# Performance work log

Hardware: AMD Instinct MI355X
Metric: run time of the kernel (lower is better)

Reference implementation:

```python
import jax, jax.numpy as jnp
import numpy as np

# Model dims (match init_kwargs)
B, S = 2, 2048
H = 1024          # hidden_size
I = 256           # intermediate_size
E = 256           # n_routed_experts
K = 8             # num_experts_per_tok
G = 8             # n_group
TG = 4            # topk_group
NS = 2            # n_shared_experts


def setup_inputs() -> dict:
    key = jax.random.key(0)
    ks = jax.random.split(key, 6)
    s = 0.02
    return {
        "x": jax.random.normal(ks[0], (B, S, H), jnp.float32),
        "Wg": jax.random.normal(ks[1], (E, H), jnp.float32) * s,          # gate Linear weight [E,H] (y = x @ Wg.T)
        "W_gate_up": jax.random.normal(ks[2], (E, H, 2 * I), jnp.float32) * s,  # per-expert gate_up proj
        "W_down": jax.random.normal(ks[3], (E, I, H), jnp.float32) * s,          # per-expert down proj
        "Ws_gate_up": jax.random.normal(ks[4], (NS, H, 2 * I), jnp.float32) * s, # shared experts
        "Ws_down": jax.random.normal(ks[5], (NS, I, H), jnp.float32) * s,
    }


def _mlp(x, w_gu, w_d):
    # DeepSeekV3 MLP: down( silu(gate) * up ); gate/up are the two chunks of gate_up
    gu = x @ w_gu                      # [N, 2I]
    g, u = gu[..., :I], gu[..., I:]
    return (jax.nn.silu(g) * u) @ w_d  # [N, H]


def reference(x, Wg, W_gate_up, W_down, Ws_gate_up, Ws_down):
    b, s, h = x.shape
    xf = x.reshape(-1, h)              # [N, H]
    n = xf.shape[0]

    # ---- shared experts (always active, averaged) ----
    shared = (_mlp(xf, Ws_gate_up[0], Ws_down[0]) + _mlp(xf, Ws_gate_up[1], Ws_down[1])) / NS

    # ---- grouped top-k gating ----
    logits = xf @ Wg.T                               # [N, E]
    gsize = E // G
    gl = logits.reshape(n, G, gsize)                 # [N, G, gsize]
    g_top_l, g_top_i = jax.lax.top_k(gl, TG)         # top-TG within each group
    cand_l = g_top_l.reshape(n, G * TG)              # candidate logits (group-major)
    cand_i = g_top_i.reshape(n, G * TG)              # within-group expert ids
    top_l, pos = jax.lax.top_k(cand_l, K)            # global top-K over candidates
    topk_idx = (pos // TG) * gsize + jnp.take_along_axis(cand_i, pos, axis=1)  # [N, K]
    topk_w = jax.nn.softmax(top_l, axis=-1)          # [N, K]

    # ---- routed experts: sort-by-expert + grouped GEMM (ragged_dot) ----
    flat_idx = topk_idx.reshape(-1)                  # [N*K]
    flat_w = topk_w.reshape(-1)
    order = jnp.argsort(flat_idx)                    # tokens grouped by expert id
    tok = order // K                                 # source token of each assignment
    xs = xf[tok]                                     # [N*K, H] gathered tokens, expert-contiguous
    gsz = jnp.bincount(flat_idx, length=E).astype(jnp.int32)  # tokens per expert

    gu = jax.lax.ragged_dot(xs, W_gate_up, gsz)      # [N*K, 2I] grouped GEMM 1
    hmid = jax.nn.silu(gu[:, :I]) * gu[:, I:]
    yo = jax.lax.ragged_dot(hmid, W_down, gsz)       # [N*K, H] grouped GEMM 2
    yo = yo * flat_w[order][:, None]                 # weight by gate prob

    routed = jnp.zeros_like(xf).at[tok].add(yo)      # scatter-add combine

    return (shared + routed).reshape(b, s, h)
```

## Files before the change

kernel.cpp:

```cpp
#include <hip/hip_runtime.h>
#include <hip/hip_bf16.h>


typedef __attribute__((ext_vector_type(4))) float  f32x4;
typedef __attribute__((ext_vector_type(8))) short  bf16x8;
typedef __attribute__((ext_vector_type(4))) short  bf16x4;
typedef __attribute__((ext_vector_type(4))) unsigned short u16x4;

#define DI static __device__ __forceinline__

DI unsigned short f2bf(float f){
  unsigned u = __builtin_bit_cast(unsigned, f);
  return (unsigned short)((u + 0x7FFFu + ((u>>16)&1u)) >> 16);
}
DI float bf2f(unsigned short s){
  return __builtin_bit_cast(float, ((unsigned)s)<<16);
}

#define WS_XBF      0u
#define WS_HSH      8388608u
#define WS_HMID     12582912u
#define WS_YSLOT    29360128u
#define WS_TOPKI    96468992u
#define WS_TOPKW    96600064u
#define WS_TOKMAP   96731136u
#define WS_SLOTMAP  96862208u
#define WS_CNT      96993280u
#define WS_CURSOR   96994304u
#define WS_ZERO     96995328u
#define WS_OFF      96999424u

__global__ void k_convert(const float* __restrict__ x, unsigned short* __restrict__ xbf){
  size_t i = ((size_t)blockIdx.x*256 + threadIdx.x)*8;
  f32x4 v0 = *(const f32x4*)(x+i), v1 = *(const f32x4*)(x+i+4);
  u16x4 a, b;
  a[0]=f2bf(v0[0]); a[1]=f2bf(v0[1]); a[2]=f2bf(v0[2]); a[3]=f2bf(v0[3]);
  b[0]=f2bf(v1[0]); b[1]=f2bf(v1[1]); b[2]=f2bf(v1[2]); b[3]=f2bf(v1[3]);
  *(u16x4*)(xbf+i) = a; *(u16x4*)(xbf+i+4) = b;
}

__global__ __launch_bounds__(256) void k_router(const float* __restrict__ x, const float* __restrict__ Wg,
                                                int* __restrict__ topki, float* __restrict__ topkw,
                                                int* __restrict__ cnt){
  __shared__ float xs[8][1024];
  __shared__ float lg[8][256];
  __shared__ float cv[8][32];
  __shared__ int   ce[8][32];
  const int tid = threadIdx.x;
  const int t0  = blockIdx.x * 8;
  {
    const f32x4* xg = (const f32x4*)(x + (size_t)t0*1024);
    f32x4* xs4 = (f32x4*)&xs[0][0];
    #pragma unroll
    for (int i=0;i<8;++i) xs4[tid + i*256] = xg[tid + i*256];
  }
  __syncthreads();
  {
    const f32x4* wg4 = (const f32x4*)(Wg + (size_t)tid*1024);
    f32x4 a[8];
    #pragma unroll
    for (int t=0;t<8;++t) a[t] = (f32x4){0.f,0.f,0.f,0.f};
    for (int i=0;i<256;++i){
      f32x4 w = wg4[i];
      #pragma unroll
      for (int t=0;t<8;++t) a[t] += w * ((const f32x4*)&xs[t][0])[i];
    }
    #pragma unroll
    for (int t=0;t<8;++t){
      double d = ((double)a[t][0] + (double)a[t][1]) + ((double)a[t][2] + (double)a[t][3]);
      lg[t][tid] = (float)d;
    }
  }
  __syncthreads();
  if (tid < 64){
    int tok = tid>>3, grp = tid&7;
    unsigned mask = 0;
    for (int j=0;j<4;++j){
      float best = -3.4e38f; int bi = 0;
      for (int i=0;i<32;++i){
        float v = lg[tok][grp*32+i];
        if (!((mask>>i)&1u) && v > best){ best=v; bi=i; }
      }
      mask |= 1u<<bi;
      cv[tok][grp*4+j] = best; ce[tok][grp*4+j] = grp*32+bi;
    }
  }
  __syncthreads();
  if (tid < 8){
    int tok = tid; unsigned mask=0;
    float vals[8]; int es[8];
    #pragma unroll
    for (int k=0;k<8;++k){
      float best=-3.4e38f; int bp=0;
      for (int p=0;p<32;++p){
        float v = cv[tok][p];
        if (!((mask>>p)&1u) && v > best){ best=v; bp=p; }
      }
      mask|=1u<<bp; vals[k]=best; es[k]=ce[tok][bp];
    }
    float m = vals[0], s=0.f, w[8];
    #pragma unroll
    for (int k=0;k<8;++k){ w[k]=expf(vals[k]-m); s+=w[k]; }
    float inv = 1.f/s;
    #pragma unroll
    for (int k=0;k<8;++k){
      int g=(t0+tok)*8+k;
      topki[g]=es[k]; topkw[g]=w[k]*inv;
      atomicAdd(&cnt[es[k]],1);
    }
  }
}

__global__ void k_scan(const int* __restrict__ cnt, int* __restrict__ off){
  __shared__ int s[256];
  int tid=threadIdx.x;
  s[tid]=cnt[tid]; __syncthreads();
  for (int d=1; d<256; d<<=1){
    int v = (tid>=d)? s[tid-d] : 0; __syncthreads();
    s[tid]+=v; __syncthreads();
  }
  off[tid+1]=s[tid]; if(tid==0) off[0]=0;
}

__global__ void k_scatter(const int* __restrict__ topki, const int* __restrict__ off,
                          int* __restrict__ cursor, int* __restrict__ tokmap, int* __restrict__ slotmap){
  int g = blockIdx.x*256 + threadIdx.x;
  int e = topki[g];
  int p = off[e] + atomicAdd(&cursor[e], 1);
  tokmap[p] = g >> 3;
  slotmap[g] = p;
}

template<int GEMM>
__global__ __launch_bounds__(512, 2) void k_gemm(
    const unsigned short* __restrict__ A1, const unsigned short* __restrict__ A2,
    const float* __restrict__ WE, const float* __restrict__ WS,
    const int* __restrict__ cnt, const int* __restrict__ off,
    const int* __restrict__ tokmap,
    unsigned short* __restrict__ O1, unsigned short* __restrict__ O2,
    float* __restrict__ OD, const unsigned short* __restrict__ zpage)
{
  __shared__ __align__(16) char smem[98304];
  const int e = blockIdx.x, mt = blockIdx.y, nc = blockIdx.z;
  const bool sh = (e >= 256);
  const int M = sh ? 4096 : cnt[e];
  const int Moff = mt*256;
  if (Moff >= M) return;
  const int tid=threadIdx.x, ln=tid&63, wv=tid>>6, wm=wv>>2, wn=wv&3, lrow=ln&15, lk=ln>>4;
  const int Ktot = (GEMM==1)?1024:(sh?512:256);
  const int ldB  = (GEMM==1)?512:1024;
  const float* Bp = (GEMM==1) ? (sh? WS + (size_t)(e-256)*524288 : WE + (size_t)e*524288)
                              : (sh? WS : WE + (size_t)e*262144);
  const int offe = sh? 0 : off[e];

  const char* a_src[2];
  #pragma unroll
  for (int qi=0;qi<2;++qi){
    int row  = (wv*2+qi)*16 + (ln>>2);
    int grow = Moff + row;
    const unsigned short* p;
    if (GEMM==1){
      if (!sh) p = (grow < M)? A1 + (size_t)tokmap[offe+grow]*1024 : zpage;
      else     p = A1 + (size_t)grow*1024;
    } else {
      if (!sh) p = (grow < M)? A1 + ((size_t)offe+grow)*256 : zpage;
      else     p = A2 + (size_t)grow*512;
    }
    a_src[qi] = (const char*)p + (ln&3)*16;
  }
  const char* b_src[4];
  {
    int swz = ((wv>>1)&3)<<2;
    int cg  = ln ^ swz;
    int tcb = cg*4;
    int gcol = (GEMM==1)? (nc*128 + tcb + ((tcb>=128)?128:0)) : (nc*256 + tcb);
    #pragma unroll
    for (int r=0;r<4;++r){
      int kr = wv*4 + r;
      b_src[r] = (const char*)(Bp + (size_t)kr*ldB + gcol);
    }
  }

  f32x4 acc[8][4] = {};

  auto stage = [&](int buf, int k0){
    #pragma unroll
    for (int qi=0;qi<2;++qi)
      __builtin_amdgcn_global_load_lds((const void*)(a_src[qi] + (size_t)k0*2),
          (void*)(smem + buf*16384 + (wv*2+qi)*1024), 16, 0, 0);
    #pragma unroll
    for (int r=0;r<4;++r)
      __builtin_amdgcn_global_load_lds((const void*)(b_src[r] + (size_t)k0*ldB*4),
          (void*)(smem + 32768 + buf*32768 + (wv*4+r)*1024), 16, 0, 0);
  };

  auto compute = [&](int buf){
    const short* as  = (const short*)(smem + buf*16384);
    const float* bs  = (const float*)(smem + 32768 + buf*32768);
    bf16x8 af[8];
    #pragma unroll
    for (int mi=0;mi<8;++mi) af[mi] = *(const bf16x8*)(as + (wm*128+mi*16+lrow)*32 + lk*8);
    #pragma unroll
    for (int ni=0;ni<4;++ni){
      int n0 = (GEMM==1)? ((ni<2)? wn*32+ni*16 : 128+wn*32+(ni-2)*16) : (wn*64+ni*16);
      int tc = n0 + lrow;
      int sloff = ((((tc>>2) ^ (lk<<2))<<2) | (tc&3));
      const float* colp = bs + (size_t)lk*8*256 + sloff;
      bf16x8 bv;
      #pragma unroll
      for (int j=0;j<8;++j){
        unsigned u = __builtin_bit_cast(unsigned, colp[(size_t)j*256]);
        bv[j] = (short)((u + 0x8000u) >> 16);
      }
      #pragma unroll
      for (int mi=0;mi<8;++mi)
        acc[mi][ni] = __builtin_amdgcn_mfma_f32_16x16x32_bf16(af[mi], bv, acc[mi][ni], 0,0,0);
    }
  };

  stage(0, 0);
  const int ns = Ktot>>5;
  for (int t=0;t<ns;++t){
    int b = t&1;
    if (t+1<ns){
      stage(b^1, (t+1)<<5);
      asm volatile("s_waitcnt vmcnt(6)" ::: "memory");
    } else {
      asm volatile("s_waitcnt vmcnt(0)" ::: "memory");
    }
    asm volatile("s_barrier" ::: "memory");
    compute(b);
    asm volatile("s_barrier" ::: "memory");
  }

  if (GEMM==1){
    __syncthreads();
    unsigned short* Hs = (unsigned short*)smem;
    #pragma unroll
    for (int mi=0;mi<8;++mi)
      #pragma unroll
      for (int ni=0;ni<2;++ni){
        f32x4 g = acc[mi][ni], u = acc[mi][ni+2];
        #pragma unroll
        for (int r=0;r<4;++r){
          float gg = g[r];
          float hh = (gg / (1.f + __expf(-gg))) * u[r];
          int m = wm*128 + mi*16 + lk*4 + r;
          int c = wn*32 + ni*16 + lrow;
          Hs[m*128 + c] = f2bf(hh);
        }
      }
    __syncthreads();
    #pragma unroll
    for (int i=0;i<8;++i){
      int id = tid + i*512, m = id>>4, c8 = id&15;
      int grow = Moff + m;
      if (grow < M){
        unsigned short* dst = (!sh) ? O1 + ((size_t)offe + grow)*256 + nc*128 + c8*8
                                    : O2 + (size_t)grow*512 + (size_t)(e-256)*256 + nc*128 + c8*8;
        *(f32x4*)dst = *(const f32x4*)(Hs + m*128 + c8*8);
      }
    }
  } else {
    if (sh){
      #pragma unroll
      for (int mi=0;mi<8;++mi)
        #pragma unroll
        for (int ni=0;ni<4;++ni)
          #pragma unroll
          for (int r=0;r<4;++r){
            int m = Moff + wm*128 + mi*16 + lk*4 + r;
            int c = nc*256 + wn*64 + ni*16 + lrow;
            OD[(size_t)m*1024 + c] = acc[mi][ni][r]*0.5f;
          }
    } else {
      unsigned short* Hs = (unsigned short*)smem;
      #pragma unroll
      for (int pass=0; pass<2; ++pass){
        __syncthreads();
        if ((wn>>1) == pass){
          #pragma unroll
          for (int mi=0;mi<8;++mi)
            #pragma unroll
            for (int ni=0;ni<4;++ni)
              #pragma unroll
              for (int r=0;r<4;++r){
                int m = wm*128 + mi*16 + lk*4 + r;
                int c = (wn&1)*64 + ni*16 + lrow;
                Hs[m*128 + c] = f2bf(acc[mi][ni][r]);
              }
        }
        __syncthreads();
        #pragma unroll
        for (int i=0;i<8;++i){
          int id = tid + i*512, m = id>>4, c8 = id&15;
          int grow = Moff + m;
          if (grow < M){
            unsigned short* dst = O1 + ((size_t)offe+grow)*1024 + nc*256 + pass*128 + c8*8;
            *(f32x4*)dst = *(const f32x4*)(Hs + m*128 + c8*8);
          }
        }
      }
    }
  }
}

__global__ void k_final(float* __restrict__ out, const unsigned short* __restrict__ yslot,
                        const int* __restrict__ slotmap, const float* __restrict__ topkw){
  __shared__ int sp[8]; __shared__ float sw[8];
  int t = blockIdx.x, tid = threadIdx.x;
  if (tid<8){ sp[tid]=slotmap[t*8+tid]; sw[tid]=topkw[t*8+tid]; }
  __syncthreads();
  int c = tid*4;
  f32x4 o = *(f32x4*)(out + (size_t)t*1024 + c);
  #pragma unroll
  for (int k=0;k<8;++k){
    u16x4 y = *(const u16x4*)(yslot + (size_t)sp[k]*1024 + c);
    float w = sw[k];
    o[0] += w*bf2f(y[0]); o[1] += w*bf2f(y[1]); o[2] += w*bf2f(y[2]); o[3] += w*bf2f(y[3]);
  }
  *(f32x4*)(out + (size_t)t*1024 + c) = o;
}

extern "C" void kernel_launch(void* const* d_in, const int* in_sizes, int n_in,
                              void* d_out, int out_size, void* d_ws, size_t ws_size,
                              hipStream_t stream) {
  const float* x    = (const float*)d_in[0];
  const float* Wg   = (const float*)d_in[1];
  const float* Wgu  = (const float*)d_in[2];
  const float* Wd   = (const float*)d_in[3];
  const float* Wsgu = (const float*)d_in[4];
  const float* Wsd  = (const float*)d_in[5];
  float* out = (float*)d_out;

  char* W = (char*)d_ws;
  unsigned short* xbf    = (unsigned short*)(W + WS_XBF);
  unsigned short* hsh    = (unsigned short*)(W + WS_HSH);
  unsigned short* hmid   = (unsigned short*)(W + WS_HMID);
  unsigned short* yslot  = (unsigned short*)(W + WS_YSLOT);
  int*   topki   = (int*)(W + WS_TOPKI);
  float* topkw   = (float*)(W + WS_TOPKW);
  int*   tokmap  = (int*)(W + WS_TOKMAP);
  int*   slotmap = (int*)(W + WS_SLOTMAP);
  int*   cnt     = (int*)(W + WS_CNT);
  int*   cursor  = (int*)(W + WS_CURSOR);
  unsigned short* zpage = (unsigned short*)(W + WS_ZERO);
  int*   off     = (int*)(W + WS_OFF);

  hipMemsetAsync((void*)cnt, 0, 1024+1024+4096, stream);

  k_router <<<512, 256, 0, stream>>>(x, Wg, topki, topkw, cnt);
  k_convert<<<2048, 256, 0, stream>>>(x, xbf);
  k_scan   <<<1, 256, 0, stream>>>(cnt, off);
  k_scatter<<<128, 256, 0, stream>>>(topki, off, cursor, tokmap, slotmap);
  k_gemm<1><<<dim3(258,16,2), 512, 0, stream>>>(xbf, (const unsigned short*)nullptr,
        Wgu, Wsgu, cnt, off, tokmap, hmid, hsh, out, zpage);
  k_gemm<2><<<dim3(257,16,4), 512, 0, stream>>>(hmid, hsh,
        Wd, Wsd, cnt, off, tokmap, yslot, (unsigned short*)nullptr, out, zpage);
  k_final <<<4096, 256, 0, stream>>>(out, yslot, slotmap, topkw);
}
```

Before: 427.8 us.

## Fuse combine into down-GEMM via atomics, triple-buffer loads, compact grid, transpose router weights

```diff
diff --git a/kernel.cpp b/kernel.cpp
--- a/kernel.cpp
+++ b/kernel.cpp
@@ -20,26 +20,36 @@
 #define WS_XBF      0u
 #define WS_HSH      8388608u
 #define WS_HMID     12582912u
-#define WS_YSLOT    29360128u
-#define WS_TOPKI    96468992u
-#define WS_TOPKW    96600064u
-#define WS_TOKMAP   96731136u
-#define WS_SLOTMAP  96862208u
-#define WS_CNT      96993280u
-#define WS_CURSOR   96994304u
-#define WS_ZERO     96995328u
-#define WS_OFF      96999424u
-
-__global__ void k_convert(const float* __restrict__ x, unsigned short* __restrict__ xbf){
-  size_t i = ((size_t)blockIdx.x*256 + threadIdx.x)*8;
-  f32x4 v0 = *(const f32x4*)(x+i), v1 = *(const f32x4*)(x+i+4);
-  u16x4 a, b;
-  a[0]=f2bf(v0[0]); a[1]=f2bf(v0[1]); a[2]=f2bf(v0[2]); a[3]=f2bf(v0[3]);
-  b[0]=f2bf(v1[0]); b[1]=f2bf(v1[1]); b[2]=f2bf(v1[2]); b[3]=f2bf(v1[3]);
-  *(u16x4*)(xbf+i) = a; *(u16x4*)(xbf+i+4) = b;
-}
-
-__global__ __launch_bounds__(256) void k_router(const float* __restrict__ x, const float* __restrict__ Wg,
+#define WS_WGT      29360128u
+#define WS_TOPKI    30408704u
+#define WS_TOPKW    30539776u
+#define WS_TOKMAP   30670848u
+#define WS_WMAP     30801920u
+#define WS_CNT      30932992u
+#define WS_CURSOR   30934016u
+#define WS_ZERO     30935040u
+#define WS_OFF      30939136u
+
+__global__ __launch_bounds__(256) void k_wgT(const float* __restrict__ Wg, float* __restrict__ WgT){
+  __shared__ float t[64][65];
+  const int tid = threadIdx.x;
+  const int hx = blockIdx.x * 64;
+  const int ex = blockIdx.y * 64;
+  #pragma unroll
+  for (int k=0;k<16;++k){
+    int i = (tid>>6)*16 + k, j = tid&63;
+    t[i][j] = Wg[(size_t)(ex+i)*1024 + hx + j];
+  }
+  __syncthreads();
+  #pragma unroll
+  for (int k=0;k<16;++k){
+    int i = (tid>>6)*16 + k, j = tid&63;
+    WgT[(size_t)(hx+i)*256 + ex + j] = t[j][i];
+  }
+}
+
+__global__ __launch_bounds__(256) void k_router(const float* __restrict__ x, const float* __restrict__ WgT,
+                                                unsigned short* __restrict__ xbf,
                                                 int* __restrict__ topki, float* __restrict__ topkw,
                                                 int* __restrict__ cnt){
   __shared__ float xs[8][1024];
@@ -51,23 +61,36 @@
   {
     const f32x4* xg = (const f32x4*)(x + (size_t)t0*1024);
     f32x4* xs4 = (f32x4*)&xs[0][0];
-    #pragma unroll
-    for (int i=0;i<8;++i) xs4[tid + i*256] = xg[tid + i*256];
+    u16x4* xb4 = (u16x4*)(xbf + (size_t)t0*1024);
+    #pragma unroll
+    for (int i=0;i<8;++i){
+      f32x4 v = xg[tid + i*256];
+      xs4[tid + i*256] = v;
+      u16x4 p; p[0]=f2bf(v[0]); p[1]=f2bf(v[1]); p[2]=f2bf(v[2]); p[3]=f2bf(v[3]);
+      xb4[tid + i*256] = p;
+    }
   }
   __syncthreads();
   {
-    const f32x4* wg4 = (const f32x4*)(Wg + (size_t)tid*1024);
-    f32x4 a[8];
-    #pragma unroll
-    for (int t=0;t<8;++t) a[t] = (f32x4){0.f,0.f,0.f,0.f};
-    for (int i=0;i<256;++i){
-      f32x4 w = wg4[i];
-      #pragma unroll
-      for (int t=0;t<8;++t) a[t] += w * ((const f32x4*)&xs[t][0])[i];
+    f32x4 a4[8];
+    #pragma unroll
+    for (int t=0;t<8;++t) a4[t] = (f32x4){0.f,0.f,0.f,0.f};
+    const float* wc = WgT + tid;
+    for (int h4=0; h4<256; ++h4){
+      float w0 = wc[(size_t)(h4*4+0)*256];
+      float w1 = wc[(size_t)(h4*4+1)*256];
+      float w2 = wc[(size_t)(h4*4+2)*256];
+      float w3 = wc[(size_t)(h4*4+3)*256];
+      f32x4 wv = (f32x4){w0,w1,w2,w3};
+      #pragma unroll
+      for (int t=0;t<8;++t){
+        f32x4 xv = *((const f32x4*)&xs[t][0] + h4);
+        a4[t] += wv * xv;
+      }
     }
     #pragma unroll
     for (int t=0;t<8;++t){
-      double d = ((double)a[t][0] + (double)a[t][1]) + ((double)a[t][2] + (double)a[t][3]);
+      double d = ((double)a4[t][0] + (double)a4[t][1]) + ((double)a4[t][2] + (double)a4[t][3]);
       lg[t][tid] = (float)d;
     }
   }
@@ -122,13 +145,14 @@
   off[tid+1]=s[tid]; if(tid==0) off[0]=0;
 }
 
-__global__ void k_scatter(const int* __restrict__ topki, const int* __restrict__ off,
-                          int* __restrict__ cursor, int* __restrict__ tokmap, int* __restrict__ slotmap){
+__global__ void k_scatter(const int* __restrict__ topki, const float* __restrict__ topkw,
+                          const int* __restrict__ off, int* __restrict__ cursor,
+                          int* __restrict__ tokmap, float* __restrict__ wmap){
   int g = blockIdx.x*256 + threadIdx.x;
   int e = topki[g];
   int p = off[e] + atomicAdd(&cursor[e], 1);
   tokmap[p] = g >> 3;
-  slotmap[g] = p;
+  wmap[p]   = topkw[g];
 }
 
 template<int GEMM>
@@ -136,12 +160,21 @@
     const unsigned short* __restrict__ A1, const unsigned short* __restrict__ A2,
     const float* __restrict__ WE, const float* __restrict__ WS,
     const int* __restrict__ cnt, const int* __restrict__ off,
-    const int* __restrict__ tokmap,
+    const int* __restrict__ tokmap, const float* __restrict__ wmap,
     unsigned short* __restrict__ O1, unsigned short* __restrict__ O2,
     float* __restrict__ OD, const unsigned short* __restrict__ zpage)
 {
-  __shared__ __align__(16) char smem[98304];
-  const int e = blockIdx.x, mt = blockIdx.y, nc = blockIdx.z;
+  __shared__ __align__(16) char smem[147456];
+  int e, mt, nc;
+  if (GEMM==1){
+    int bx = blockIdx.x;
+    if (bx < 1024){ e = bx>>2; nc = (bx>>1)&1; mt = bx&1; }
+    else { int i = bx-1024; e = 256 + (i>>5); mt = (i>>1)&15; nc = i&1; }
+  } else {
+    int bx = blockIdx.x;
+    if (bx < 2048){ e = bx>>3; nc = (bx>>1)&3; mt = bx&1; }
+    else { int i = bx-2048; e = 256; mt = i>>2; nc = i&3; }
+  }
   const bool sh = (e >= 256);
   const int M = sh ? 4096 : cnt[e];
   const int Moff = mt*256;
@@ -191,12 +224,12 @@
     #pragma unroll
     for (int r=0;r<4;++r)
       __builtin_amdgcn_global_load_lds((const void*)(b_src[r] + (size_t)k0*ldB*4),
-          (void*)(smem + 32768 + buf*32768 + (wv*4+r)*1024), 16, 0, 0);
+          (void*)(smem + 49152 + buf*32768 + (wv*4+r)*1024), 16, 0, 0);
   };
 
   auto compute = [&](int buf){
     const short* as  = (const short*)(smem + buf*16384);
-    const float* bs  = (const float*)(smem + 32768 + buf*32768);
+    const float* bs  = (const float*)(smem + 49152 + buf*32768);
     bf16x8 af[8];
     #pragma unroll
     for (int mi=0;mi<8;++mi) af[mi] = *(const bf16x8*)(as + (wm*128+mi*16+lrow)*32 + lk*8);
@@ -218,19 +251,24 @@
     }
   };
 
+  const int ns = Ktot>>5;
   stage(0, 0);
-  const int ns = Ktot>>5;
+  if (ns>1) stage(1, 32);
+  int bt = 0;
   for (int t=0;t<ns;++t){
-    int b = t&1;
-    if (t+1<ns){
-      stage(b^1, (t+1)<<5);
+    if (t+2<ns){
+      int bn = bt+2; if (bn>=3) bn-=3;
+      stage(bn, (t+2)<<5);
+      asm volatile("s_waitcnt vmcnt(12)" ::: "memory");
+    } else if (t+1<ns){
       asm volatile("s_waitcnt vmcnt(6)" ::: "memory");
     } else {
       asm volatile("s_waitcnt vmcnt(0)" ::: "memory");
     }
     asm volatile("s_barrier" ::: "memory");
-    compute(b);
+    compute(bt);
     asm volatile("s_barrier" ::: "memory");
+    ++bt; if (bt==3) bt=0;
   }
 
   if (GEMM==1){
@@ -271,55 +309,31 @@
           for (int r=0;r<4;++r){
             int m = Moff + wm*128 + mi*16 + lk*4 + r;
             int c = nc*256 + wn*64 + ni*16 + lrow;
-            OD[(size_t)m*1024 + c] = acc[mi][ni][r]*0.5f;
+            atomicAdd(&OD[(size_t)m*1024 + c], acc[mi][ni][r]*0.5f);
           }
     } else {
-      unsigned short* Hs = (unsigned short*)smem;
-      #pragma unroll
-      for (int pass=0; pass<2; ++pass){
-        __syncthreads();
-        if ((wn>>1) == pass){
+      __syncthreads();
+      int*   stok = (int*)smem;
+      float* swgt = (float*)(smem + 2048);
+      if (tid < 256){
+        int gr = Moff + tid;
+        if (gr < M){ stok[tid] = tokmap[offe+gr]; swgt[tid] = wmap[offe+gr]; }
+      }
+      __syncthreads();
+      #pragma unroll
+      for (int mi=0;mi<8;++mi)
+        #pragma unroll
+        for (int ni=0;ni<4;++ni)
           #pragma unroll
-          for (int mi=0;mi<8;++mi)
-            #pragma unroll
-            for (int ni=0;ni<4;++ni)
-              #pragma unroll
-              for (int r=0;r<4;++r){
-                int m = wm*128 + mi*16 + lk*4 + r;
-                int c = (wn&1)*64 + ni*16 + lrow;
-                Hs[m*128 + c] = f2bf(acc[mi][ni][r]);
-              }
-        }
-        __syncthreads();
-        #pragma unroll
-        for (int i=0;i<8;++i){
-          int id = tid + i*512, m = id>>4, c8 = id&15;
-          int grow = Moff + m;
-          if (grow < M){
-            unsigned short* dst = O1 + ((size_t)offe+grow)*1024 + nc*256 + pass*128 + c8*8;
-            *(f32x4*)dst = *(const f32x4*)(Hs + m*128 + c8*8);
+          for (int r=0;r<4;++r){
+            int lr = wm*128 + mi*16 + lk*4 + r;
+            if (Moff + lr < M){
+              int c = nc*256 + wn*64 + ni*16 + lrow;
+              atomicAdd(&OD[(size_t)stok[lr]*1024 + c], swgt[lr]*acc[mi][ni][r]);
+            }
           }
-        }
-      }
-    }
-  }
-}
-
-__global__ void k_final(float* __restrict__ out, const unsigned short* __restrict__ yslot,
-                        const int* __restrict__ slotmap, const float* __restrict__ topkw){
-  __shared__ int sp[8]; __shared__ float sw[8];
-  int t = blockIdx.x, tid = threadIdx.x;
-  if (tid<8){ sp[tid]=slotmap[t*8+tid]; sw[tid]=topkw[t*8+tid]; }
-  __syncthreads();
-  int c = tid*4;
-  f32x4 o = *(f32x4*)(out + (size_t)t*1024 + c);
-  #pragma unroll
-  for (int k=0;k<8;++k){
-    u16x4 y = *(const u16x4*)(yslot + (size_t)sp[k]*1024 + c);
-    float w = sw[k];
-    o[0] += w*bf2f(y[0]); o[1] += w*bf2f(y[1]); o[2] += w*bf2f(y[2]); o[3] += w*bf2f(y[3]);
-  }
-  *(f32x4*)(out + (size_t)t*1024 + c) = o;
+    }
+  }
 }
 
 extern "C" void kernel_launch(void* const* d_in, const int* in_sizes, int n_in,
@@ -337,25 +351,25 @@
   unsigned short* xbf    = (unsigned short*)(W + WS_XBF);
   unsigned short* hsh    = (unsigned short*)(W + WS_HSH);
   unsigned short* hmid   = (unsigned short*)(W + WS_HMID);
-  unsigned short* yslot  = (unsigned short*)(W + WS_YSLOT);
+  float* WgT     = (float*)(W + WS_WGT);
   int*   topki   = (int*)(W + WS_TOPKI);
   float* topkw   = (float*)(W + WS_TOPKW);
   int*   tokmap  = (int*)(W + WS_TOKMAP);
-  int*   slotmap = (int*)(W + WS_SLOTMAP);
+  float* wmap    = (float*)(W + WS_WMAP);
   int*   cnt     = (int*)(W + WS_CNT);
   int*   cursor  = (int*)(W + WS_CURSOR);
   unsigned short* zpage = (unsigned short*)(W + WS_ZERO);
   int*   off     = (int*)(W + WS_OFF);
 
   hipMemsetAsync((void*)cnt, 0, 1024+1024+4096, stream);
-
-  k_router <<<512, 256, 0, stream>>>(x, Wg, topki, topkw, cnt);
-  k_convert<<<2048, 256, 0, stream>>>(x, xbf);
+  hipMemsetAsync((void*)out, 0, (size_t)out_size*4, stream);
+
+  k_wgT    <<<dim3(16,4), 256, 0, stream>>>(Wg, WgT);
+  k_router <<<512, 256, 0, stream>>>(x, WgT, xbf, topki, topkw, cnt);
   k_scan   <<<1, 256, 0, stream>>>(cnt, off);
-  k_scatter<<<128, 256, 0, stream>>>(topki, off, cursor, tokmap, slotmap);
-  k_gemm<1><<<dim3(258,16,2), 512, 0, stream>>>(xbf, (const unsigned short*)nullptr,
-        Wgu, Wsgu, cnt, off, tokmap, hmid, hsh, out, zpage);
-  k_gemm<2><<<dim3(257,16,4), 512, 0, stream>>>(hmid, hsh,
-        Wd, Wsd, cnt, off, tokmap, yslot, (unsigned short*)nullptr, out, zpage);
-  k_final <<<4096, 256, 0, stream>>>(out, yslot, slotmap, topkw);
-}
+  k_scatter<<<128, 256, 0, stream>>>(topki, topkw, off, cursor, tokmap, wmap);
+  k_gemm<1><<<1088, 512, 0, stream>>>(xbf, (const unsigned short*)nullptr,
+        Wgu, Wsgu, cnt, off, tokmap, wmap, hmid, hsh, out, zpage);
+  k_gemm<2><<<2112, 512, 0, stream>>>(hmid, hsh,
+        Wd, Wsd, cnt, off, tokmap, wmap, (unsigned short*)nullptr, (unsigned short*)nullptr, out, zpage);
+}
```

Result: slower. 555.8 us (+29.9%).
